# Kernel optimization log

Hardware: AMD Instinct MI355X
Metric: run time of the kernel (lower is better)

Reference implementation:

```python
import jax, jax.numpy as jnp
import numpy as np


def setup_inputs() -> dict:
    key = jax.random.key(0)
    k1, k2 = jax.random.split(key)
    B, T, V = 128, 256, 256
    batch = jax.random.normal(k1, (B, T, V, 3), dtype=jnp.float32)
    missing = jax.random.uniform(k2, (B, T, V)) < 0.2
    labels = jnp.where(missing, -1.0, 1.0)
    batch = batch.at[..., 0].set(labels)
    return {"batch": batch}


def reference(batch):
    B, T, V, _ = batch.shape
    dt = batch.dtype
    # constant-velocity model matrices (hardcoded in the module)
    F = jnp.array([[1, 0, 1, 0], [0, 1, 0, 1], [0, 0, 1, 0], [0, 0, 0, 1]], dtype=dt)
    H = jnp.array([[1, 0, 0, 0], [0, 1, 0, 0]], dtype=dt)
    Q = jnp.eye(4, dtype=dt) * 0.01
    R = jnp.eye(2, dtype=dt) * 1.0
    I4 = jnp.eye(4, dtype=dt)

    s0 = jnp.zeros((B, V, 4), dtype=dt)
    P0 = jnp.broadcast_to(jnp.eye(4, dtype=dt) * 1000.0, (B, V, 4, 4))

    obs_t = jnp.moveaxis(batch, 1, 0)  # (T, B, V, 3)

    def step(carry, obs):
        s, P = carry  # s: (B,V,4), P: (B,V,4,4)
        labels = obs[..., 0]
        z = obs[..., 1:]                       # (B,V,2)
        mask = (labels != -1)[..., None]       # (B,V,1)
        s_pred = jnp.einsum('bvj,ij->bvi', s, F)                 # s @ F.T
        P_pred = jnp.einsum('ij,bvjk,lk->bvil', F, P, F) + Q     # F P F^T + Q
        y = (z - s_pred[..., :2]) * mask                          # (B,V,2)
        S = P_pred[..., :2, :2] + R                               # H P H^T + R
        K = jnp.einsum('bvij,bvjk->bvik', P_pred[..., :, :2], jnp.linalg.inv(S))  # (B,V,4,2)
        s_upd = s_pred + jnp.einsum('bvij,bvj->bvi', K, y) * mask
        KH = jnp.einsum('bvij,jk->bvik', K, H)                    # (B,V,4,4)
        P_upd = jnp.einsum('bvij,bvjk->bvik', I4 - KH, P_pred)
        s_new = jnp.where(mask, s_upd, s_pred)
        P_new = jnp.where(mask[..., None], P_upd, P_pred)
        return (s_new, P_new), None

    (s_final, _), _ = jax.lax.scan(step, (s0, P0), obs_t)
    last_pos = s_final[..., :2]                                   # (B,V,2)
    ones = jnp.ones((B, V, 1), dtype=dt)
    return jnp.concatenate((ones, last_pos), axis=-1)             # (B,V,3)
```

## Files before the change

kernel.cpp:

```cpp
#include <hip/hip_runtime.h>


#define KF_B 128
#define KF_T 256
#define KF_V 256
#define KF_G 8

__global__ __launch_bounds__(64) void kf_kernel(const float* __restrict__ batch,
                                                float* __restrict__ out) {
    const int tid = blockIdx.x * 64 + threadIdx.x;
    const int b = tid >> 8;
    const int v = tid & (KF_V - 1);

    const float* __restrict__ ptr = batch + ((size_t)b * KF_T * KF_V + v) * 3;
    const int stride = KF_V * 3;

    float s0 = 0.f, s1 = 0.f, s2 = 0.f, s3 = 0.f;
    float p00 = 1000.f, p01 = 0.f, p02 = 0.f, p03 = 0.f;
    float p11 = 1000.f, p12 = 0.f, p13 = 0.f;
    float p22 = 1000.f, p23 = 0.f;
    float p33 = 1000.f;

    const float Qd = 0.01f;

    float bufA[KF_G][3], bufB[KF_G][3];

#define KF_LOAD(dst)                               \
    do {                                           \
        _Pragma("unroll")                          \
        for (int k = 0; k < KF_G; ++k) {           \
            (dst)[k][0] = ptr[k * stride + 0];     \
            (dst)[k][1] = ptr[k * stride + 1];     \
            (dst)[k][2] = ptr[k * stride + 2];     \
        }                                          \
        ptr += KF_G * stride;                      \
    } while (0)

#define KF_STEP(obs)                                                        \
    do {                                                                    \
        const float label = (obs)[0];                                       \
        const float z0 = (obs)[1];                                          \
        const float z1 = (obs)[2];                                          \
                                                               \
        const float sp0 = s0 + s2;                                          \
        const float sp1 = s1 + s3;                                          \
        const float q00 = p00 + 2.f * p02 + p22 + Qd;                       \
        const float q01 = p01 + p12 + p03 + p23;                            \
        const float q02 = p02 + p22;                                        \
        const float q03 = p03 + p23;                                        \
        const float q11 = p11 + 2.f * p13 + p33 + Qd;                       \
        const float q12 = p12 + p23;                                        \
        const float q13 = p13 + p33;                                        \
        const float q22 = p22 + Qd;                                         \
        const float q23 = p23;                                              \
        const float q33 = p33 + Qd;                                         \
                                       \
        const float S00 = q00 + 1.f;                                        \
        const float S01 = q01;                                              \
        const float S11 = q11 + 1.f;                                        \
        const float det = S00 * S11 - S01 * S01;                            \
        const float m = (label != -1.0f) ? 1.0f : 0.0f;                     \
        const float idet = m * __builtin_amdgcn_rcpf(det);                  \
        const float t0 = idet * S11;                                        \
        const float t1 = idet * S01;                                        \
        const float t2 = idet * S00;                                        \
        const float K00 = q00 * t0 - q01 * t1;                              \
        const float K01 = q01 * t2 - q00 * t1;                              \
        const float K10 = q01 * t0 - q11 * t1;                              \
        const float K11 = q11 * t2 - q01 * t1;                              \
        const float K20 = q02 * t0 - q12 * t1;                              \
        const float K21 = q12 * t2 - q02 * t1;                              \
        const float K30 = q03 * t0 - q13 * t1;                              \
        const float K31 = q13 * t2 - q03 * t1;                              \
        const float y0 = z0 - sp0;                                          \
        const float y1 = z1 - sp1;                                          \
        s0 = sp0 + K00 * y0 + K01 * y1;                                     \
        s1 = sp1 + K10 * y0 + K11 * y1;                                     \
                                  \
        s2 = s2 + K20 * y0 + K21 * y1;                                      \
        s3 = s3 + K30 * y0 + K31 * y1;                                      \
        p00 = q00 - (K00 * q00 + K01 * q01);                                \
        p01 = q01 - (K00 * q01 + K01 * q11);                                \
        p02 = q02 - (K00 * q02 + K01 * q12);                                \
        p03 = q03 - (K00 * q03 + K01 * q13);                                \
        p11 = q11 - (K10 * q01 + K11 * q11);                                \
        p12 = q12 - (K10 * q02 + K11 * q12);                                \
        p13 = q13 - (K10 * q03 + K11 * q13);                                \
        p22 = q22 - (K20 * q02 + K21 * q12);                                \
        p23 = q23 - (K20 * q03 + K21 * q13);                                \
        p33 = q33 - (K30 * q03 + K31 * q13);                                \
    } while (0)

    KF_LOAD(bufA);

    const int NG = KF_T / KF_G;
    for (int g = 0; g < NG; g += 2) {
        KF_LOAD(bufB);
#pragma unroll
        for (int k = 0; k < KF_G; ++k) KF_STEP(bufA[k]);
        if (g + 2 < NG) {
            KF_LOAD(bufA);
        }
#pragma unroll
        for (int k = 0; k < KF_G; ++k) KF_STEP(bufB[k]);
    }

    float* o = out + (size_t)tid * 3;
    o[0] = 1.0f;
    o[1] = s0;
    o[2] = s1;
}

extern "C" void kernel_launch(void* const* d_in, const int* in_sizes, int n_in,
                              void* d_out, int out_size, void* d_ws, size_t ws_size,
                              hipStream_t stream) {
    (void)in_sizes; (void)n_in; (void)d_ws; (void)ws_size; (void)out_size;
    const float* batch = (const float*)d_in[0];
    float* out = (float*)d_out;
    const int total = KF_B * KF_V;
    kf_kernel<<<total / 64, 64, 0, stream>>>(batch, out);
}
```

Before: 168.7 us.

## Decouple Kalman filter into shared 2x2 covariance per axis, enlarge prefetch group

Because P0, Q and R are scaled identities, the x and y axes evolve independently with identical covariance. The state update therefore reduces to one shared 2x2 symmetric covariance (three scalars) and a scalar innovation inverse, replacing the full 4x4 update and 2x2 matrix inverse. This cuts per-step arithmetic and register pressure substantially. The prefetch group also grows from 8 to 32 timesteps, which raises register use for the load buffers but allows more loads in flight.

Measured after the change: 147.5 us. 12.6% less time.

```diff
diff --git a/kernel.cpp b/kernel.cpp
--- a/kernel.cpp
+++ b/kernel.cpp
@@ -4,7 +4,7 @@
 #define KF_B 128
 #define KF_T 256
 #define KF_V 256
-#define KF_G 8
+#define KF_G 32
 
 __global__ __launch_bounds__(64) void kf_kernel(const float* __restrict__ batch,
                                                 float* __restrict__ out) {
@@ -15,13 +15,9 @@
     const float* __restrict__ ptr = batch + ((size_t)b * KF_T * KF_V + v) * 3;
     const int stride = KF_V * 3;
 
-    float s0 = 0.f, s1 = 0.f, s2 = 0.f, s3 = 0.f;
-    float p00 = 1000.f, p01 = 0.f, p02 = 0.f, p03 = 0.f;
-    float p11 = 1000.f, p12 = 0.f, p13 = 0.f;
-    float p22 = 1000.f, p23 = 0.f;
-    float p33 = 1000.f;
-
-    const float Qd = 0.01f;
+    float p00 = 1000.f, p01 = 0.f, p11 = 1000.f;
+    float x0 = 0.f, v0 = 0.f;
+    float x1 = 0.f, v1 = 0.f;
 
     float bufA[KF_G][3], bufB[KF_G][3];
 
@@ -36,59 +32,34 @@
         ptr += KF_G * stride;                      \
     } while (0)
 
-#define KF_STEP(obs)                                                        \
-    do {                                                                    \
-        const float label = (obs)[0];                                       \
-        const float z0 = (obs)[1];                                          \
-        const float z1 = (obs)[2];                                          \
-                                                               \
-        const float sp0 = s0 + s2;                                          \
-        const float sp1 = s1 + s3;                                          \
-        const float q00 = p00 + 2.f * p02 + p22 + Qd;                       \
-        const float q01 = p01 + p12 + p03 + p23;                            \
-        const float q02 = p02 + p22;                                        \
-        const float q03 = p03 + p23;                                        \
-        const float q11 = p11 + 2.f * p13 + p33 + Qd;                       \
-        const float q12 = p12 + p23;                                        \
-        const float q13 = p13 + p33;                                        \
-        const float q22 = p22 + Qd;                                         \
-        const float q23 = p23;                                              \
-        const float q33 = p33 + Qd;                                         \
-                                       \
-        const float S00 = q00 + 1.f;                                        \
-        const float S01 = q01;                                              \
-        const float S11 = q11 + 1.f;                                        \
-        const float det = S00 * S11 - S01 * S01;                            \
-        const float m = (label != -1.0f) ? 1.0f : 0.0f;                     \
-        const float idet = m * __builtin_amdgcn_rcpf(det);                  \
-        const float t0 = idet * S11;                                        \
-        const float t1 = idet * S01;                                        \
-        const float t2 = idet * S00;                                        \
-        const float K00 = q00 * t0 - q01 * t1;                              \
-        const float K01 = q01 * t2 - q00 * t1;                              \
-        const float K10 = q01 * t0 - q11 * t1;                              \
-        const float K11 = q11 * t2 - q01 * t1;                              \
-        const float K20 = q02 * t0 - q12 * t1;                              \
-        const float K21 = q12 * t2 - q02 * t1;                              \
-        const float K30 = q03 * t0 - q13 * t1;                              \
-        const float K31 = q13 * t2 - q03 * t1;                              \
-        const float y0 = z0 - sp0;                                          \
-        const float y1 = z1 - sp1;                                          \
-        s0 = sp0 + K00 * y0 + K01 * y1;                                     \
-        s1 = sp1 + K10 * y0 + K11 * y1;                                     \
-                                  \
-        s2 = s2 + K20 * y0 + K21 * y1;                                      \
-        s3 = s3 + K30 * y0 + K31 * y1;                                      \
-        p00 = q00 - (K00 * q00 + K01 * q01);                                \
-        p01 = q01 - (K00 * q01 + K01 * q11);                                \
-        p02 = q02 - (K00 * q02 + K01 * q12);                                \
-        p03 = q03 - (K00 * q03 + K01 * q13);                                \
-        p11 = q11 - (K10 * q01 + K11 * q11);                                \
-        p12 = q12 - (K10 * q02 + K11 * q12);                                \
-        p13 = q13 - (K10 * q03 + K11 * q13);                                \
-        p22 = q22 - (K20 * q02 + K21 * q12);                                \
-        p23 = q23 - (K20 * q03 + K21 * q13);                                \
-        p33 = q33 - (K30 * q03 + K31 * q13);                                \
+#define KF_STEP(obs)                                                    \
+    do {                                                                \
+        const float label = (obs)[0];                                   \
+        const float z0 = (obs)[1];                                      \
+        const float z1 = (obs)[2];                                      \
+                                                           \
+        const float xp0 = x0 + v0;                                      \
+        const float xp1 = x1 + v1;                                      \
+        const float q00 = p00 + 2.f * p01 + p11 + 0.01f;                \
+        const float q01 = p01 + p11;                                    \
+        const float q11 = p11 + 0.01f;                                  \
+                    \
+        const float S = q00 + 1.f;                                      \
+        const float m = (label != -1.0f) ? 1.0f : 0.0f;                 \
+        const float is = m * __builtin_amdgcn_rcpf(S);                  \
+        const float K0 = q00 * is;                                      \
+        const float K1 = q01 * is;                                      \
+                                   \
+        const float y0 = z0 - xp0;                                      \
+        const float y1 = z1 - xp1;                                      \
+        x0 = xp0 + K0 * y0;                                             \
+        v0 = v0 + K1 * y0;                                              \
+        x1 = xp1 + K0 * y1;                                             \
+        v1 = v1 + K1 * y1;                                              \
+                                                 \
+        p00 = q00 - K0 * q00;                                           \
+        p01 = q01 - K0 * q01;                                           \
+        p11 = q11 - K1 * q01;                                           \
     } while (0)
 
     KF_LOAD(bufA);
@@ -107,8 +78,8 @@
 
     float* o = out + (size_t)tid * 3;
     o[0] = 1.0f;
-    o[1] = s0;
-    o[2] = s1;
+    o[1] = x0;
+    o[2] = x1;
 }
 
 extern "C" void kernel_launch(void* const* d_in, const int* in_sizes, int n_in,
```
